# Kernel optimization log

Hardware: AMD Instinct MI355X
Metric: run time of the kernel (lower is better)

Reference implementation:

```python
import jax, jax.numpy as jnp
import numpy as np

LOG2PI = float(np.log(2.0 * np.pi))
T, DZ, DX = 512, 32, 32  # dx == dz so all quad forms stack homogeneously


def _spd(key, d):
    a = jax.random.normal(key, (d, d))
    return a @ a.T / d + jnp.eye(d)


def setup_inputs() -> dict:
    key = jax.random.key(0)
    k = jax.random.split(key, 17)
    return {
        "observations": jax.random.normal(k[0], (T, DX)),
        "m_prior_mean": jax.random.normal(k[1], (DZ,)),
        "m_prior_cov": _spd(k[2], DZ),
        "m_trans_w": 0.3 * jax.random.normal(k[3], (DZ, DZ)),
        "m_trans_b": jax.random.normal(k[4], (DZ,)),
        "m_trans_cov": _spd(k[5], DZ),
        "m_emis_w": 0.3 * jax.random.normal(k[6], (DX, DZ)),
        "m_emis_b": jax.random.normal(k[7], (DX,)),
        "m_emis_cov": _spd(k[8], DX),
        "v_prior_mean": jax.random.normal(k[9], (DZ,)),
        "v_prior_cov": _spd(k[10], DZ),
        "v_trans_w": 0.3 * jax.random.normal(k[11], (DZ, DZ)),
        "v_trans_b": jax.random.normal(k[12], (DZ,)),
        "v_trans_cov": _spd(k[13], DZ),
        "v_emis_w": 0.3 * jax.random.normal(k[14], (DX, DZ)),
        "v_emis_b": jax.random.normal(k[15], (DX,)),
        "v_emis_cov": _spd(k[16], DX),
    }


def _elbo(observations, m_prior_mean, m_prior_cov, m_trans_w, m_trans_b,
          m_trans_cov, m_emis_w, m_emis_b, m_emis_cov, v_prior_mean,
          v_prior_cov, v_trans_w, v_trans_b, v_trans_cov, v_emis_w,
          v_emis_b, v_emis_cov):
    Tn, dx = observations.shape
    dz = m_trans_cov.shape[0]
    I = jnp.eye(dz, dtype=observations.dtype)

    def logdet(M):
        return jnp.log(jnp.linalg.det(M))

    def cterm(dim, ld):  # -0.5*(dim*log(2pi) + log det)
        return -0.5 * (dim * LOG2PI + ld)

    m_trans_prec = jnp.linalg.inv(m_trans_cov)
    m_trans_ld = logdet(m_trans_cov)
    m_emis_prec = jnp.linalg.inv(m_emis_cov)
    m_emis_ld = logdet(m_emis_cov)
    v_trans_prec = jnp.linalg.inv(v_trans_cov)

    # ---- Kalman filter on the variational model ----
    def kf_update(m, P, y):
        S = v_emis_w @ P @ v_emis_w.T + v_emis_cov
        K = P @ v_emis_w.T @ jnp.linalg.inv(S)
        m2 = m + K @ (y - (v_emis_w @ m + v_emis_b))
        P2 = (I - K @ v_emis_w) @ P
        return m2, P2

    def kf_step(m, P, y):
        mp = v_trans_w @ m + v_trans_b
        Pp = v_trans_w @ P @ v_trans_w.T + v_trans_cov
        return kf_update(mp, Pp, y)

    # ---- stacked quad forms; list grows by 2 per step -> 2T slots ----
    N = 2 * Tn
    Om = jnp.zeros((N, dz, dz), observations.dtype)
    A = jnp.zeros((N, dz, dz), observations.dtype)
    b = jnp.zeros((N, dz), observations.dtype)
    # slot 0: emission/obs term at t=0
    Om = Om.at[0].set(-0.5 * m_emis_prec)
    A = A.at[0].set(m_emis_w)
    b = b.at[0].set(m_emis_b - observations[0])
    # slot 1: prior term
    Om = Om.at[1].set(-0.5 * jnp.linalg.inv(m_prior_cov))
    A = A.at[1].set(I)
    b = b.at[1].set(-m_prior_mean)

    fm, fP = kf_update(v_prior_mean, v_prior_cov, observations[0])
    c0 = cterm(dz, logdet(m_prior_cov)) + cterm(dx, m_emis_ld)

    def step(carry, xs):
        fm, fP, c, Om, A, b = carry
        t, y = xs
        # backward kernel from current filtering state
        fprec = jnp.linalg.inv(fP)
        common = v_trans_w.T @ v_trans_prec
        bcov = jnp.linalg.inv(common @ v_trans_w + fprec)
        bA = bcov @ common
        ba = bcov @ (fprec @ fm - common @ v_trans_b)
        # integrate all existing quad forms under the backward kernel
        # (zero slots contribute exactly 0, so no masking is needed)
        AbC = jnp.einsum('nij,jk->nik', A, bcov)
        c = c + jnp.sum(jnp.einsum('nab,nbc,nac->n', Om, AbC, A))
        A2 = jnp.einsum('nij,jk->nik', A, bA)
        b2 = jnp.einsum('nij,j->ni', A, ba) + b
        c = c + cterm(dx, m_emis_ld) + cterm(dz, m_trans_ld)
        # transition quad form expectation constant
        c = c - 0.5 * jnp.trace(m_trans_prec @ m_trans_w @ bcov @ m_trans_w.T)
        # append obs term (slot 2t) and transition term (slot 2t+1)
        Om2 = Om.at[2 * t].set(-0.5 * m_emis_prec).at[2 * t + 1].set(-0.5 * m_trans_prec)
        A2 = A2.at[2 * t].set(m_emis_w).at[2 * t + 1].set(m_trans_w @ bA - I)
        b2 = b2.at[2 * t].set(m_emis_b - y).at[2 * t + 1].set(m_trans_w @ ba + m_trans_b)
        # backward entropy constant + 0.5*dz
        c = c - cterm(dz, logdet(bcov)) + 0.5 * dz
        fm2, fP2 = kf_step(fm, fP, y)
        return (fm2, fP2, c, Om2, A2, b2), None

    ts = jnp.arange(1, Tn)
    (fm, fP, c, Om, A, b), _ = jax.lax.scan(
        step, (fm, fP, c0, Om, A, b), (ts, observations[1:]))

    # final expectations under the filtering distribution
    c = c - cterm(dz, logdet(fP))
    # trace(Omega @ A @ fP @ A)  -- note A (not A.T), faithful to the source
    tr = jnp.einsum('nab,nbc,cd,nda->n', Om, A, fP, A)
    cm = jnp.einsum('nij,j->ni', A, fm) + b
    qf = jnp.einsum('ni,nij,nj->n', cm, Om, cm)
    c = c + jnp.sum(tr) + jnp.sum(qf) + 0.5 * dz
    return c


def reference(observations, m_prior_mean, m_prior_cov, m_trans_w, m_trans_b,
              m_trans_cov, m_emis_w, m_emis_b, m_emis_cov, v_prior_mean,
              v_prior_cov, v_trans_w, v_trans_b, v_trans_cov, v_emis_w,
              v_emis_b, v_emis_cov):
    return _elbo(observations, m_prior_mean, m_prior_cov, m_trans_w,
                 m_trans_b, m_trans_cov, m_emis_w, m_emis_b, m_emis_cov,
                 v_prior_mean, v_prior_cov, v_trans_w, v_trans_b,
                 v_trans_cov, v_emis_w, v_emis_b, v_emis_cov)
```

## Files before the change

### kernel.cpp

```cpp
#include <hip/hip_runtime.h>
#include <math.h>

#define TT 512
#define CH 8
#define NCH 64
#define NB 128
#define NGRP 8
#define GSZ (NB/NGRP)
#define ST 36
#define MS 1152
#define LOG2PI 1.8378770664093453

static_assert(TT == CH * NCH, "chunking");

enum : int {
  WS_X     = 0,
  WS_BCOV  = WS_X    + TT*1024,
  WS_BA    = WS_BCOV + TT*1024,
  WS_YT    = WS_BA   + TT*32,
  WS_MTP   = WS_YT   + TT*32,
  WS_MEP   = WS_MTP + 1024,
  WS_MPP   = WS_MEP + 1024,
  WS_QI    = WS_MPP + 1024,
  WS_RI    = WS_QI  + 1024,
  WS_P0I   = WS_RI  + 1024,
  WS_QIW   = WS_P0I + 1024,
  WS_CW    = WS_QIW + 1024,
  WS_HTRI  = WS_CW  + 1024,
  WS_HTRIH = WS_HTRI+ 1024,
  WS_TQ    = WS_HTRIH+1024,
  WS_EM    = WS_TQ  + 1024,
  WS_EML   = WS_EM  + 1024,
  WS_LAM0CW= WS_EML + 1024,
  WS_QHC   = WS_LAM0CW + 1024,
  WS_C1    = WS_QHC + 1024,
  WS_EMM   = WS_C1  + 1024,
  WS_S1    = WS_EMM + 1024,
  WS_FPT   = WS_S1  + 1024,
  WS_ETA0  = WS_FPT + 1024,
  WS_CTB   = WS_ETA0 + 32,
  WS_QIVTB = WS_CTB + 32,
  WS_FMT   = WS_QIVTB + 32,
  WS_ETAF  = WS_FMT + 32,
  WS_LDS3  = WS_ETAF + 32,
  WS_DACC  = WS_LDS3 + 4,
  WS_Z512  = WS_DACC + 8,
  WS_OPS   = WS_Z512 + 1024,
  WS_GBAR  = WS_OPS + 6*3072,
  WS_PART  = WS_GBAR + 4352,
  WS_ETA_A = WS_PART + 416,
  WS_ETA_B = WS_ETA_A + NCH*1056,
  WS_CEA   = WS_ETA_B + NCH*1056,
  WS_CEB   = WS_CEA + NCH*2048,
  WS_END   = WS_CEB + NCH*2048
};
static_assert(WS_DACC % 2 == 0 && WS_PART % 2 == 0, "double alignment");

__device__ __forceinline__ float rlane(float v, int l) {
  return __uint_as_float(__builtin_amdgcn_readlane(__float_as_uint(v), l));
}
__device__ __forceinline__ float dot4(const float4 a, const float4 b) {
  return a.x*b.x + a.y*b.y + a.z*b.z + a.w*b.w;
}

__device__ __forceinline__ double gj_inv32(float a[32]) {
  double pp = 1.0;
#pragma unroll
  for (int p = 0; p < 32; ++p) {
    const float piv = rlane(a[p], p);
    pp *= (double)piv;
    const float sc = a[p] * (1.0f / piv);
#pragma unroll
    for (int r = 0; r < 32; ++r) {
      if (r != p) a[r] -= rlane(a[r], p) * sc;
    }
    a[p] = sc;
  }
  return pp;
}

__device__ __forceinline__ double wave_inv36(float* M, int tid) {
  float a[32]; const int cc = tid & 31;
#pragma unroll
  for (int r = 0; r < 32; ++r)
    a[r] = (tid < 32) ? M[r*ST + cc] : ((r == tid - 32) ? 1.f : 0.f);
  const double pp = gj_inv32(a);
  if (tid >= 32) {
    const int c2 = tid - 32;
#pragma unroll
    for (int r = 0; r < 32; ++r) M[r*ST + c2] = a[r];
  }
  return pp;
}

__device__ __forceinline__ float block_reduce(float v, float* red, int tid) {
#pragma unroll
  for (int m = 32; m >= 1; m >>= 1) v += __shfl_xor(v, m, 64);
  if ((tid & 63) == 0) red[tid >> 6] = v;
  __syncthreads();
  return red[0] + red[1] + red[2] + red[3];
}

__device__ __forceinline__ void stage_mat(const float* __restrict__ g, float* L, int tid) {
  const int r = tid >> 3, c = (tid & 7) * 4;
  *(float4*)(L + r*ST + c) = *(const float4*)(g + r*32 + c);
}
__device__ __forceinline__ void destage_mat(const float* L, float* __restrict__ g, int tid) {
  const int r = tid >> 3, c = (tid & 7) * 4;
  *(float4*)(g + r*32 + c) = *(const float4*)(L + r*ST + c);
}

__device__ __forceinline__ void mm_rr(const float* A, const float* B, float* C, int tid) {
  const int j = tid & 31, r0 = tid >> 5;
  float4 b[8];
#pragma unroll
  for (int kk = 0; kk < 8; ++kk) b[kk] = *(const float4*)(B + j*ST + 4*kk);
#pragma unroll
  for (int m = 0; m < 4; ++m) {
    const int ri = r0 + 8*m;
    float s = 0.f;
#pragma unroll
    for (int kk = 0; kk < 8; ++kk)
      s += dot4(*(const float4*)(A + ri*ST + 4*kk), b[kk]);
    C[ri*ST+j] = s;
  }
}
__device__ __forceinline__ void mm_rr_sub(const float* A, const float* B,
                                          const float* Base, float* C, int tid) {
  const int j = tid & 31, r0 = tid >> 5;
  float4 b[8];
#pragma unroll
  for (int kk = 0; kk < 8; ++kk) b[kk] = *(const float4*)(B + j*ST + 4*kk);
#pragma unroll
  for (int m = 0; m < 4; ++m) {
    const int ri = r0 + 8*m;
    float s = 0.f;
#pragma unroll
    for (int kk = 0; kk < 8; ++kk)
      s += dot4(*(const float4*)(A + ri*ST + 4*kk), b[kk]);
    C[ri*ST+j] = Base[ri*ST+j] - s;
  }
}
__device__ __forceinline__ void mm_rr_subg(const float* A, const float* B,
                                           const float* __restrict__ gBase,
                                           float* C, int tid) {
  const int j = tid & 31, r0 = tid >> 5;
  float4 b[8];
#pragma unroll
  for (int kk = 0; kk < 8; ++kk) b[kk] = *(const float4*)(B + j*ST + 4*kk);
#pragma unroll
  for (int m = 0; m < 4; ++m) {
    const int ri = r0 + 8*m;
    float s = 0.f;
#pragma unroll
    for (int kk = 0; kk < 8; ++kk)
      s += dot4(*(const float4*)(A + ri*ST + 4*kk), b[kk]);
    C[ri*ST+j] = gBase[ri*32+j] - s;
  }
}
__device__ __forceinline__ void mm_p(const float* A, const float* B, float* C, int tid) {
  const int ri = tid >> 3, j4 = (tid & 7) * 4;
  float4 acc = {0.f,0.f,0.f,0.f};
#pragma unroll 8
  for (int k = 0; k < 32; ++k) {
    const float a = A[ri*ST + k];
    const float4 b = *(const float4*)(B + k*ST + j4);
    acc.x += a*b.x; acc.y += a*b.y; acc.z += a*b.z; acc.w += a*b.w;
  }
  *(float4*)(C + ri*ST + j4) = acc;
}
__device__ __forceinline__ void mm_p_sub(const float* A, const float* B,
                                         const float* Base, float* C, int tid) {
  const int ri = tid >> 3, j4 = (tid & 7) * 4;
  float4 acc = *(const float4*)(Base + ri*ST + j4);
#pragma unroll 8
  for (int k = 0; k < 32; ++k) {
    const float a = A[ri*ST + k];
    const float4 b = *(const float4*)(B + k*ST + j4);
    acc.x -= a*b.x; acc.y -= a*b.y; acc.z -= a*b.z; acc.w -= a*b.w;
  }
  *(float4*)(C + ri*ST + j4) = acc;
}
__device__ __forceinline__ void mm_tp(const float* A, const float* B, float* C, int tid) {
  const int ri = tid >> 3, j4 = (tid & 7) * 4;
  float4 acc = {0.f,0.f,0.f,0.f};
#pragma unroll 8
  for (int k = 0; k < 32; ++k) {
    const float a = A[k*ST + ri];
    const float4 b = *(const float4*)(B + k*ST + j4);
    acc.x += a*b.x; acc.y += a*b.y; acc.z += a*b.z; acc.w += a*b.w;
  }
  *(float4*)(C + ri*ST + j4) = acc;
}
__device__ __forceinline__ void mm_tp_addL(const float* A, const float* B,
                                           const float* AddL, float* C, int tid) {
  const int ri = tid >> 3, j4 = (tid & 7) * 4;
  float4 acc = *(const float4*)(AddL + ri*ST + j4);
#pragma unroll 8
  for (int k = 0; k < 32; ++k) {
    const float a = A[k*ST + ri];
    const float4 b = *(const float4*)(B + k*ST + j4);
    acc.x += a*b.x; acc.y += a*b.y; acc.z += a*b.z; acc.w += a*b.w;
  }
  *(float4*)(C + ri*ST + j4) = acc;
}

__device__ __forceinline__ void gridbar(unsigned* base, int idx, int blk) {
  __syncthreads();
  if (threadIdx.x == 0) {
    const int g = blk & (NGRP-1);
    unsigned* lcl  = base + idx*128 + g*16;
    unsigned* go   = base + 2048 + idx*128 + g*16;
    unsigned* glob = base + 4096 + idx*16;
    __threadfence();
    __hip_atomic_fetch_add(lcl, 1u, __ATOMIC_RELEASE, __HIP_MEMORY_SCOPE_AGENT);
    if (blk < NGRP) {
      while (__hip_atomic_load(lcl, __ATOMIC_ACQUIRE, __HIP_MEMORY_SCOPE_AGENT)
             < (unsigned)GSZ)
        __builtin_amdgcn_s_sleep(1);
      __hip_atomic_fetch_add(glob, 1u, __ATOMIC_RELEASE, __HIP_MEMORY_SCOPE_AGENT);
      while (__hip_atomic_load(glob, __ATOMIC_ACQUIRE, __HIP_MEMORY_SCOPE_AGENT)
             < (unsigned)NGRP)
        __builtin_amdgcn_s_sleep(1);
      __hip_atomic_store(go, 1u, __ATOMIC_RELEASE, __HIP_MEMORY_SCOPE_AGENT);
    } else {
      while (__hip_atomic_load(go, __ATOMIC_ACQUIRE, __HIP_MEMORY_SCOPE_AGENT) == 0u)
        __builtin_amdgcn_s_sleep(1);
    }
  }
  __syncthreads();
}

__device__ void dev_k2(const float* __restrict__ obs, const float* __restrict__ vpm,
                       const float* __restrict__ vtw, const float* __restrict__ vtb,
                       const float* __restrict__ vew, const float* __restrict__ veb,
                       const float* __restrict__ mtw, const float* __restrict__ mew,
                       float* __restrict__ ws, int tid) {
  const int j = tid & 31, r0 = tid >> 5;
#pragma unroll
  for (int m = 0; m < 4; ++m) {
    const int ri = r0 + 8*m;
    float s1 = 0.f, s2 = 0.f, s3 = 0.f, s4 = 0.f;
    for (int k = 0; k < 32; ++k) {
      s1 += ws[WS_QI  + ri*32 + k] * vtw[k*32 + j];
      s2 += vew[k*32 + ri] * ws[WS_RI + k*32 + j];
      s3 += ws[WS_MTP + ri*32 + k] * mtw[k*32 + j];
      s4 += ws[WS_MEP + ri*32 + k] * mew[k*32 + j];
    }
    ws[WS_QIW + ri*32 + j] = s1;
    ws[WS_HTRI + ri*32 + j] = s2;
    ws[WS_FPT + ri*32 + j] = s3;
    ws[WS_EML + ri*32 + j] = -0.5f * s4;
  }
  __syncthreads();
#pragma unroll
  for (int m = 0; m < 4; ++m) {
    const int ri = r0 + 8*m;
    float s1 = 0.f, s2 = 0.f, s3 = 0.f, s4 = 0.f;
    for (int k = 0; k < 32; ++k) {
      s1 += vtw[k*32 + ri] * ws[WS_QIW + k*32 + j];
      s2 += ws[WS_HTRI + ri*32 + k] * vew[k*32 + j];
      s3 += mtw[k*32 + ri] * ws[WS_FPT + k*32 + j];
      s4 += mew[k*32 + ri] * ws[WS_EML + k*32 + j];
    }
    ws[WS_CW + ri*32 + j] = s1;
    ws[WS_HTRIH + ri*32 + j] = s2;
    ws[WS_LAM0CW + ri*32 + j] = ws[WS_P0I + ri*32 + j] + s1 + s2;
    ws[WS_QHC    + ri*32 + j] = ws[WS_QI  + ri*32 + j] + s1 + s2;
    ws[WS_TQ + ri*32 + j] = s3;
    ws[WS_EM + ri*32 + j] = s4;
    ws[WS_S1 + ri*32 + j] = s4 - 0.5f * ws[WS_MPP + ri*32 + j];
    ws[WS_C1 + ri*32 + j] = ws[WS_FPT + j*32 + ri];
    ws[WS_EMM + ri*32 + j] = s4 - 0.5f * ws[WS_MTP + ri*32 + j];
  }
  if (tid < 32) {
    float s1 = 0.f, s2 = 0.f, s3 = 0.f;
    for (int k = 0; k < 32; ++k) {
      s1 += ws[WS_QIW + k*32 + tid] * vtb[k];
      s2 += ws[WS_P0I + tid*32 + k] * vpm[k]
          + ws[WS_HTRI + tid*32 + k] * (obs[k] - veb[k]);
      s3 += ws[WS_QI + tid*32 + k] * vtb[k];
    }
    ws[WS_CTB + tid] = s1;
    ws[WS_ETA0 + tid] = s2;
    ws[WS_QIVTB + tid] = s3;
  }
  __syncthreads();
  if (tid == 0) {
    const double ldmt = (double)ws[WS_LDS3 + 0];
    const double ldme = (double)ws[WS_LDS3 + 1];
    const double ldmp = (double)ws[WS_LDS3 + 2];
    const double ct_me = -0.5 * (32.0 * LOG2PI + ldme);
    const double ct_mt = -0.5 * (32.0 * LOG2PI + ldmt);
    const double ct_mp = -0.5 * (32.0 * LOG2PI + ldmp);
    double c = ct_mp + ct_me;
    c += (double)(TT - 1) * (ct_me + ct_mt + 0.5 * 32.0 * LOG2PI + 16.0);
    c += 0.5 * 32.0 * LOG2PI + 16.0;
    ((double*)(ws + WS_DACC))[0] = c;
  }
  __syncthreads();
}

__device__ void dev_compose(float* __restrict__ ws, float* sm, int tid) {
  float *Kc = sm,      *Ac = sm+MS,   *Gc = sm+2*MS;
  float *Kn = sm+3*MS, *An = sm+4*MS, *Gn = sm+5*MS;
  float *Mi = sm+6*MS, *V1 = sm+7*MS, *Wm = sm+8*MS;
  stage_mat(ws + WS_QHC, Kc, tid);
  stage_mat(ws + WS_QIW, Ac, tid);
  for (int e = tid; e < MS; e += 256) Gc[e] = 0.f;
  __syncthreads();
  for (int d = 0; d < 8; ++d) {
    for (int e = tid; e < MS; e += 256) Mi[e] = Kc[e] + Gc[e];
    __syncthreads();
    if (tid < 64) wave_inv36(Mi, tid);
    __syncthreads();
    mm_rr(Ac, Mi, V1, tid);
    mm_tp(Ac, Mi, Wm, tid);
    __syncthreads();
    mm_rr_sub(V1, Ac, Kc, Kn, tid);
    mm_p(V1, Ac, An, tid);
    mm_p_sub(Wm, Ac, Gc, Gn, tid);
    __syncthreads();
    float* tp;
    tp=Kc; Kc=Kn; Kn=tp;  tp=Ac; Ac=An; An=tp;  tp=Gc; Gc=Gn; Gn=tp;
    if (d >= 2) {
      float* op = ws + WS_OPS + (d-2)*3072;
      destage_mat(Kc, op, tid);
      destage_mat(Ac, op + 1024, tid);
      destage_mat(Gc, op + 2048, tid);
    }
  }
}

__device__ void dev_keta_a(float* __restrict__ ws, float* sm, int tid, int c) {
  float *Aa = sm, *Ab = sm+MS, *Xl = sm+2*MS, *bb = sm+3*MS;
  const int t1 = CH*c + 1;
  stage_mat(ws + WS_X + t1*1024, Aa, tid);
  if (tid < 32) bb[tid] = ws[WS_YT + t1*32 + tid];
  __syncthreads();
  float *Acur = Aa, *Anew = Ab; int pb = 0;
  for (int t = t1 + 1; t <= t1 + CH - 1; ++t) {
    stage_mat(ws + WS_X + t*1024, Xl, tid);
    __syncthreads();
    mm_p(Xl, Acur, Anew, tid);
    if (tid < 32) {
      float s = ws[WS_YT + t*32 + tid];
      for (int k = 0; k < 32; ++k) s += Xl[tid*ST+k] * bb[pb*32 + k];
      bb[(pb^1)*32 + tid] = s;
    }
    __syncthreads();
    float* tp = Acur; Acur = Anew; Anew = tp; pb ^= 1;
  }
  float* dst = ws + WS_ETA_A + (c+1)*1056;
  destage_mat(Acur, dst, tid);
  if (tid < 32) dst[1024 + tid] = bb[pb*32 + tid];
}

__device__ void dev_eta_lvl8(float* __restrict__ ws, float* sm, int tid, int c) {
  const float* in = ws + WS_ETA_A;
  float* out = ws + WS_ETA_B;
  float *AR0 = sm, *AR1 = sm+MS, *A0 = sm+2*MS;
  float *bv = sm+3*MS, *b0 = bv + 64;
  stage_mat(in + c*1056, AR0, tid);
  if (tid < 32) bv[tid] = in[c*1056 + 1024 + tid];
  __syncthreads();
  float *AR = AR0, *At = AR1; int pb = 0;
  for (int kk = 1; kk <= 7; ++kk) {
    const int idx = c - kk;
    if (idx < 0) break;
    stage_mat(in + idx*1056, A0, tid);
    if (tid < 32) b0[tid] = in[idx*1056 + 1024 + tid];
    __syncthreads();
    mm_p(AR, A0, At, tid);
    if (tid < 32) {
      float s = bv[pb*32 + tid];
      for (int k = 0; k < 32; ++k) s += AR[tid*ST+k] * b0[k];
      bv[(pb^1)*32 + tid] = s;
    }
    __syncthreads();
    float* tp = AR; AR = At; At = tp; pb ^= 1;
  }
  destage_mat(AR, out + c*1056, tid);
  if (tid < 32) out[c*1056 + 1024 + tid] = bv[pb*32 + tid];
}

__device__ void dev_keta_b(float* __restrict__ ws, float* sm, int tid, int c) {
  float *A_0 = sm, *A_1 = sm+MS, *A_2 = sm+2*MS;
  float *bb = sm+3*MS;
  stage_mat(ws + WS_ETA_B + c*1056, A_0, tid);
  if (tid < 32) bb[tid] = ws[WS_ETA_B + c*1056 + 1024 + tid];
  __syncthreads();
  float *AR = A_0, *Ax = A_1; int pb = 0;
  for (int kk = 1; kk <= 7; ++kk) {
    const int idx = c - 8*kk;
    if (idx < 0) break;
    stage_mat(ws + WS_ETA_B + idx*1056, A_2, tid);
    if (tid < 32) bb[64 + tid] = ws[WS_ETA_B + idx*1056 + 1024 + tid];
    __syncthreads();
    mm_p(AR, A_2, Ax, tid);
    if (tid < 32) {
      float s = bb[pb*32 + tid];
      for (int k = 0; k < 32; ++k) s += AR[tid*ST+k] * bb[64+k];
      bb[(pb^1)*32 + tid] = s;
    }
    __syncthreads();
    float* tp = AR; AR = Ax; Ax = tp; pb ^= 1;
  }
  float *zeta = bb + 96, *zn = bb + 128;
  if (tid < 32) {
    float s = bb[pb*32 + tid];
    for (int k = 0; k < 32; ++k)
      s += AR[tid*ST+k] * (ws[WS_ETA0 + k] - ws[WS_CTB + k]);
    zeta[tid] = s;
  }
  __syncthreads();
  float *Bl = A_0, *Xl = A_1;
  const int nst = (c == NCH-1) ? CH-1 : CH;
  for (int i = 0; i < nst; ++i) {
    const int t = CH*c + 1 + i;
    stage_mat(ws + WS_BCOV + t*1024, Bl, tid);
    stage_mat(ws + WS_X + t*1024, Xl, tid);
    __syncthreads();
    if (tid < 32) {
      float s = 0.f;
      for (int k = 0; k < 32; ++k) s += Bl[tid*ST+k] * zeta[k];
      ws[WS_BA + t*32 + tid] = s;
    } else if (tid < 64) {
      const int i2 = tid - 32;
      float s = ws[WS_YT + t*32 + i2];
      for (int k = 0; k < 32; ++k) s += Xl[i2*ST+k] * zeta[k];
      zn[i2] = s;
    }
    __syncthreads();
    if (tid < 32) zeta[tid] = zn[tid];
    __syncthreads();
  }
  if (c == NCH-1 && tid < 32)
    ws[WS_ETAF + tid] = zeta[tid] + ws[WS_CTB + tid];
}

__device__ void dev_ksa(float* __restrict__ ws, float* sm, int tid, int c) {
  float *BTa=sm,      *BTb=sm+MS,   *Ka=sm+2*MS,  *Kb=sm+3*MS,
        *Tk=sm+4*MS,  *XC1=sm+5*MS, *Xl=sm+6*MS,  *KmTQ=sm+7*MS,
        *TQl=sm+8*MS, *EMMl=sm+9*MS,*C1l=sm+10*MS;
  const int t1 = CH*c + 1, t2 = CH*c + CH;
  const int j = tid & 31, r0 = tid >> 5;
  stage_mat(ws + WS_TQ, TQl, tid);
  stage_mat(ws + WS_EMM, EMMl, tid);
  stage_mat(ws + WS_C1, C1l, tid);
  for (int e = tid; e < MS; e += 256) {
    const int r = e / ST, cc = e - ST*r;
    BTa[e] = (cc < 32 && cc == r) ? 1.f : 0.f;
    Ka[e] = 0.f;
  }
  __syncthreads();
  float *BTc = BTa, *BTn = BTb, *Kc = Ka, *Kn = Kb;
  for (int t = t1; t <= t2; ++t) {
    stage_mat(ws + WS_X + t*1024, Xl, tid);
    for (int e = tid; e < MS; e += 256) KmTQ[e] = Kc[e] - 0.5f * TQl[e];
    __syncthreads();
    mm_rr(BTc, Xl, BTn, tid);
    mm_rr(Xl, KmTQ, Tk, tid);
    mm_p(Xl, C1l, XC1, tid);
    __syncthreads();
    {
      float4 xb[8];
#pragma unroll
      for (int kk = 0; kk < 8; ++kk) xb[kk] = *(const float4*)(Xl + j*ST + 4*kk);
#pragma unroll
      for (int m = 0; m < 4; ++m) {
        const int ri = r0 + 8*m;
        float s = 0.f;
#pragma unroll
        for (int kk = 0; kk < 8; ++kk)
          s += dot4(*(const float4*)(Tk + ri*ST + 4*kk), xb[kk]);
        Kn[ri*ST+j] = s + 0.5f*(XC1[ri*ST+j] + XC1[j*ST+ri]) + EMMl[ri*ST+j];
      }
    }
    __syncthreads();
    float* tp = BTc; BTc = BTn; BTn = tp;
    tp = Kc; Kc = Kn; Kn = tp;
  }
  float* dst = ws + WS_CEA + (c+1)*2048;
  destage_mat(BTc, dst, tid);
  destage_mat(Kc, dst + 1024, tid);
}

__device__ void dev_ks_lvl8(float* __restrict__ ws, float* sm, int tid, int c) {
  const float* in = ws + WS_CEA;
  float* out = ws + WS_CEB;
  float *BT0=sm, *BT1=sm+MS, *K0=sm+2*MS, *K1=sm+3*MS,
        *BTo=sm+4*MS, *Ko=sm+5*MS, *tmp=sm+6*MS;
  stage_mat(in + c*2048, BT0, tid);
  stage_mat(in + c*2048 + 1024, K0, tid);
  __syncthreads();
  float *BTR=BT0, *BTt=BT1, *KR=K0, *Kt=K1;
  for (int kk = 1; kk <= 7; ++kk) {
    const int idx = c - kk;
    if (idx < 0) break;
    stage_mat(in + idx*2048, BTo, tid);
    stage_mat(in + idx*2048 + 1024, Ko, tid);
    __syncthreads();
    mm_p(Ko, BTR, tmp, tid);
    mm_p(BTo, BTR, BTt, tid);
    __syncthreads();
    mm_tp_addL(BTR, tmp, KR, Kt, tid);
    __syncthreads();
    float* tp = BTR; BTR = BTt; BTt = tp;
    tp = KR; KR = Kt; Kt = tp;
  }
  destage_mat(BTR, out + c*2048, tid);
  destage_mat(KR, out + c*2048 + 1024, tid);
}

__device__ void dev_ksc(float* __restrict__ ws, float* sm, float* red,
                        int tid, int c) {
  float *BT0=sm, *BT1=sm+MS, *K0=sm+2*MS, *K1=sm+3*MS,
        *BTo=sm+4*MS, *Ko=sm+5*MS, *tmp=sm+6*MS;
  stage_mat(ws + WS_CEB + c*2048, BT0, tid);
  stage_mat(ws + WS_CEB + c*2048 + 1024, K0, tid);
  __syncthreads();
  float *BTR=BT0, *BTt=BT1, *KR=K0, *Kt=K1;
  for (int kk = 1; kk <= 7; ++kk) {
    const int idx = c - 8*kk;
    if (idx < 0) break;
    stage_mat(ws + WS_CEB + idx*2048, BTo, tid);
    stage_mat(ws + WS_CEB + idx*2048 + 1024, Ko, tid);
    __syncthreads();
    mm_p(Ko, BTR, tmp, tid);
    mm_p(BTo, BTR, BTt, tid);
    __syncthreads();
    mm_tp_addL(BTR, tmp, KR, Kt, tid);
    __syncthreads();
    float* tp = BTR; BTR = BTt; BTt = tp;
    tp = KR; KR = Kt; Kt = tp;
  }
  float *TQl=sm+7*MS, *EMMl=sm+8*MS, *C1l=sm+9*MS,
        *S=sm+10*MS, *SmTQ=sm+11*MS, *XC1=sm+12*MS;
  float *T1=tmp, *Xl=BTo, *Bcl=Ko;
  const int j = tid & 31, r0 = tid >> 5;
  stage_mat(ws + WS_TQ, TQl, tid);
  stage_mat(ws + WS_EMM, EMMl, tid);
  stage_mat(ws + WS_C1, C1l, tid);
  stage_mat(ws + WS_S1, SmTQ, tid);
  __syncthreads();
  mm_p(SmTQ, BTR, T1, tid);
  __syncthreads();
  mm_tp_addL(BTR, T1, KR, S, tid);
  __syncthreads();
  double accd = 0.0;
  for (int i = 0; i < CH; ++i) {
    const int t = CH*c + 1 + i;
    if (t >= TT) break;
    stage_mat(ws + WS_X + t*1024, Xl, tid);
    stage_mat(ws + WS_BCOV + t*1024, Bcl, tid);
#pragma unroll
    for (int m = 0; m < 4; ++m) {
      const int ri = r0 + 8*m;
      SmTQ[ri*ST+j] = S[ri*ST+j] - 0.5f * TQl[ri*ST+j];
    }
    __syncthreads();
    float part = 0.f;
#pragma unroll
    for (int m = 0; m < 4; ++m) {
      const int ri = r0 + 8*m;
      part += SmTQ[ri*ST+j] * Bcl[ri*ST+j];
    }
    const float r2 = block_reduce(part, red, tid);
    if (tid == 0) accd += (double)r2;
    mm_rr(Xl, SmTQ, T1, tid);
    mm_p(Xl, C1l, XC1, tid);
    __syncthreads();
    {
      float4 xb[8];
#pragma unroll
      for (int kk = 0; kk < 8; ++kk) xb[kk] = *(const float4*)(Xl + j*ST + 4*kk);
#pragma unroll
      for (int m = 0; m < 4; ++m) {
        const int ri = r0 + 8*m;
        float s = 0.f;
#pragma unroll
        for (int kk = 0; kk < 8; ++kk)
          s += dot4(*(const float4*)(T1 + ri*ST + 4*kk), xb[kk]);
        S[ri*ST+j] = s + 0.5f*(XC1[ri*ST+j] + XC1[j*ST+ri]) + EMMl[ri*ST+j];
      }
    }
    __syncthreads();
  }
  if (tid == 0) ((double*)(ws + WS_PART))[64 + c] = accd;
}

__device__ void dev_kga(float* __restrict__ ws, float* sm, int tid, int c) {
  float *ATa = sm, *ATb = sm+MS, *Xl = sm+2*MS, *bb = sm+3*MS;
  const int t1 = CH*c + 1;
  const int t2 = (CH*c + CH < TT) ? CH*c + CH : TT - 1;
  stage_mat(ws + WS_X + t2*1024, ATa, tid);
  if (tid < 32) bb[tid] = ws[WS_BA + t2*32 + tid];
  __syncthreads();
  float *ATc = ATa, *ATn = ATb;
  int pb = 0;
  for (int t = t2 - 1; t >= t1; --t) {
    stage_mat(ws + WS_X + t*1024, Xl, tid);
    __syncthreads();
    mm_p(ATc, Xl, ATn, tid);
    if (tid < 32) {
      float s = ws[WS_BA + t*32 + tid];
      for (int k = 0; k < 32; ++k) s += Xl[k*ST+tid] * bb[pb*32 + k];
      bb[(pb^1)*32 + tid] = s;
    }
    __syncthreads();
    float* tp = ATc; ATc = ATn; ATn = tp; pb ^= 1;
  }
  float* dst = ws + WS_CEA + (c-1)*1056;
  destage_mat(ATc, dst, tid);
  if (tid < 32) dst[1024 + tid] = bb[pb*32 + tid];
}

__device__ void dev_kg_lvl8(float* __restrict__ ws, float* sm, int tid, int c) {
  const float* in = ws + WS_CEA;
  float* out = ws + WS_CEB;
  float *AR0 = sm, *AR1 = sm+MS, *ATl = sm+2*MS;
  float *bv = sm+3*MS, *bl = bv + 64;
  stage_mat(in + c*1056, AR0, tid);
  if (tid < 32) bv[tid] = in[c*1056 + 1024 + tid];
  __syncthreads();
  float *AR = AR0, *At = AR1; int pb = 0;
  for (int kk = 1; kk <= 7; ++kk) {
    const int idx = c + kk;
    if (idx > NCH - 1) break;
    stage_mat(in + idx*1056, ATl, tid);
    if (tid < 32) bl[tid] = in[idx*1056 + 1024 + tid];
    __syncthreads();
    mm_p(ATl, AR, At, tid);
    if (tid < 32) {
      float s = bv[pb*32 + tid];
      for (int k = 0; k < 32; ++k) s += AR[k*ST+tid] * bl[k];
      bv[(pb^1)*32 + tid] = s;
    }
    __syncthreads();
    float* tp = AR; AR = At; At = tp; pb ^= 1;
  }
  destage_mat(AR, out + c*1056, tid);
  if (tid < 32) out[c*1056 + 1024 + tid] = bv[pb*32 + tid];
}

__device__ void dev_kgb(const float* __restrict__ obs, const float* __restrict__ mpm,
                        const float* __restrict__ mtw, const float* __restrict__ mtb,
                        const float* __restrict__ mew, const float* __restrict__ meb,
                        float* __restrict__ ws, float* sm, float* red, int tid, int c) {
  float *ATa=sm,      *ATb=sm+MS,    *Xl=sm+2*MS,  *Y1=sm+3*MS,  *Y2=sm+4*MS,
        *Jb=sm+5*MS,  *M2T=sm+6*MS,  *mewl=sm+7*MS,*EmLl=sm+8*MS,
        *fPl=sm+9*MS, *Mtpl=sm+10*MS,*Mepl=sm+11*MS,*mtwl=sm+12*MS;
  float *vec = sm + 13*MS;
  float *fml=vec, *mebl=vec+32, *mtbl=vec+64, *mpml=vec+96, *yl=vec+128,
        *bal=vec+160, *gv=vec+192, *cme=vec+224, *cmo=vec+256, *bv=vec+288;
  const int j = tid & 31, r0 = tid >> 5;
  stage_mat(mew, mewl, tid);
  stage_mat(ws + WS_EML, EmLl, tid);
  stage_mat(ws + WS_FPT, fPl, tid);
  stage_mat(ws + WS_MTP, Mtpl, tid);
  stage_mat(ws + WS_MEP, Mepl, tid);
  stage_mat(mtw, mtwl, tid);
  stage_mat(ws + WS_CEB + c*1056, ATa, tid);
  if (tid < 32) {
    fml[tid] = ws[WS_FMT + tid];
    mebl[tid] = meb[tid]; mtbl[tid] = mtb[tid]; mpml[tid] = mpm[tid];
    bv[tid] = ws[WS_CEB + c*1056 + 1024 + tid];
  }
  __syncthreads();
  float *ATc = ATa, *ATo = ATb;
  int bc = 0;
  for (int kk = 1; kk <= 7; ++kk) {
    const int idx = c + 8*kk;
    if (idx > NCH - 1) break;
    stage_mat(ws + WS_CEB + idx*1056, Xl, tid);
    if (tid < 32) bal[tid] = ws[WS_CEB + idx*1056 + 1024 + tid];
    __syncthreads();
    mm_p(Xl, ATc, ATo, tid);
    if (tid < 32) {
      float s = bv[bc*32 + tid];
      for (int k = 0; k < 32; ++k) s += ATc[k*ST+tid] * bal[k];
      bv[(bc^1)*32 + tid] = s;
    }
    __syncthreads();
    float* tp = ATc; ATc = ATo; ATo = tp; bc ^= 1;
  }
  double accd = 0.0;
  for (int s = CH*c + CH - 1; s >= CH*c; --s) {
    if (s < TT-1) stage_mat(ws + WS_X + (s+1)*1024, Xl, tid);
    if (s == 0)   stage_mat(ws + WS_MPP, Jb, tid);
    if (tid < 32) {
      yl[tid] = obs[s*32 + tid];
      if (s >= 1) bal[tid] = ws[WS_BA + s*32 + tid];
    }
    __syncthreads();
    if (s < TT-1) {
      mm_p(ATc, Xl, ATo, tid);
      if (tid < 32) {
        float v = ws[WS_BA + (s+1)*32 + tid];
        for (int k = 0; k < 32; ++k) v += Xl[k*ST+tid] * bv[bc*32 + k];
        bv[(bc^1)*32 + tid] = v;
      }
    }
    __syncthreads();
    const float* AT = (s < TT-1) ? ATo : ATc;
    const float* bl = (s < TT-1) ? (bv + (bc^1)*32) : (bv + bc*32);
    mm_rr(mewl, AT, Y1, tid);
    mm_rr(EmLl, AT, Y2, tid);
    if (s >= 1) {
      const float* Xg = ws + WS_X + s*1024;
      float4 xg[8];
#pragma unroll
      for (int kk = 0; kk < 8; ++kk) xg[kk] = *(const float4*)(Xg + j*32 + 4*kk);
#pragma unroll
      for (int m = 0; m < 4; ++m) {
        const int ri = r0 + 8*m;
        float v = 0.f;
#pragma unroll
        for (int kk = 0; kk < 8; ++kk)
          v += dot4(*(const float4*)(mtwl + ri*ST + 4*kk), xg[kk]);
        Jb[ri*ST+j] = v - ((ri == j) ? 1.f : 0.f);
      }
    }
    if (tid < 32) {
      float g = bl[tid];
      for (int k = 0; k < 32; ++k) g += AT[k*ST+tid] * fml[k];
      gv[tid] = g;
    }
    __syncthreads();
    if (s >= 1) mm_rr(AT, Jb, M2T, tid);
    if (tid < 32) {
      float s1v = mebl[tid] - yl[tid];
      for (int k = 0; k < 32; ++k) s1v += mewl[tid*ST+k] * gv[k];
      cme[tid] = s1v;
      float s2v;
      if (s >= 1) {
        s2v = mtbl[tid];
        for (int k = 0; k < 32; ++k)
          s2v += Jb[tid*ST+k] * gv[k] + mtwl[tid*ST+k] * bal[k];
      } else {
        s2v = gv[tid] - mpml[tid];
      }
      cmo[tid] = s2v;
    }
    __syncthreads();
    const float* M2Tp = (s >= 1) ? M2T : AT;
    const float* Mqp  = (s >= 1) ? Mtpl : Jb;
    float4 fb[8], m2b[8];
#pragma unroll
    for (int kk = 0; kk < 8; ++kk) {
      fb[kk]  = *(const float4*)(fPl + j*ST + 4*kk);
      m2b[kk] = *(const float4*)(M2Tp + j*ST + 4*kk);
    }
    float part = 0.f;
#pragma unroll
    for (int m = 0; m < 4; ++m) {
      const int ri = r0 + 8*m;
      float y3 = 0.f, e2 = 0.f, e1 = 0.f;
#pragma unroll
      for (int kk = 0; kk < 8; ++kk) {
        y3 += dot4(*(const float4*)(Y2 + ri*ST + 4*kk), fb[kk]);
        e2 += dot4(fb[kk], *(const float4*)(M2Tp + ri*ST + 4*kk));
        e1 += dot4(*(const float4*)(Mqp + ri*ST + 4*kk), m2b[kk]);
      }
      part += y3 * Y1[j*ST+ri]
            - 0.5f * e1 * e2
            - 0.5f * cme[ri] * Mepl[ri*ST+j] * cme[j]
            - 0.5f * cmo[ri] * Mqp[ri*ST+j] * cmo[j];
    }
    const float r2 = block_reduce(part, red, tid);
    if (tid == 0) accd += (double)r2;
    if (s < TT-1) { float* tp = ATc; ATc = ATo; ATo = tp; bc ^= 1; }
    __syncthreads();
  }
  if (tid == 0) ((double*)(ws + WS_PART))[128 + c] = accd;
}

__global__ __launch_bounds__(256) void k0_init(float* __restrict__ ws) {
  unsigned* b = (unsigned*)(ws + WS_GBAR);
  for (int e = threadIdx.x; e < 4352; e += 256) b[e] = 0u;
}

__global__ __launch_bounds__(256) void mega(
    const float* __restrict__ obs, const float* __restrict__ mpm,
    const float* __restrict__ mpc, const float* __restrict__ mtw,
    const float* __restrict__ mtb, const float* __restrict__ mtc,
    const float* __restrict__ mew, const float* __restrict__ meb,
    const float* __restrict__ mec, const float* __restrict__ vpm,
    const float* __restrict__ vpc, const float* __restrict__ vtw,
    const float* __restrict__ vtb, const float* __restrict__ vtc,
    const float* __restrict__ vew, const float* __restrict__ veb,
    const float* __restrict__ vcc, float* __restrict__ ws,
    float* __restrict__ out) {
  __shared__ __align__(16) float sm[15360];
  __shared__ float red[4];
  const int tid = threadIdx.x, blk = blockIdx.x;
  unsigned* bars = (unsigned*)(ws + WS_GBAR);
  double* P = (double*)(ws + WS_PART);
  int bix = 0;

  if (blk < 6) {
    const float* src = blk==0?mtc : blk==1?mec : blk==2?mpc : blk==3?vtc : blk==4?vcc : vpc;
    float* dst = ws + (blk==0?WS_MTP : blk==1?WS_MEP : blk==2?WS_MPP :
                       blk==3?WS_QI  : blk==4?WS_RI  : WS_P0I);
    if (tid < 64) {
      float a[32]; const int cc = tid & 31;
#pragma unroll
      for (int r = 0; r < 32; ++r)
        a[r] = (tid < 32) ? src[r*32 + cc] : ((r == tid - 32) ? 1.f : 0.f);
      const double pp = gj_inv32(a);
      if (tid >= 32) {
        const int c2 = tid - 32;
#pragma unroll
        for (int r = 0; r < 32; ++r) dst[r*32 + c2] = a[r];
      }
      if (tid == 0 && blk < 3) ws[WS_LDS3 + blk] = (float)log(pp);
    }
  }
  gridbar(bars, bix++, blk);

  if (blk == 0) {
    dev_k2(obs, vpm, vtw, vtb, vew, veb, mtw, mew, ws, tid);
    dev_compose(ws, sm, tid);
  }
  gridbar(bars, bix++, blk);

  if (blk < NCH) {
    float *Zl=sm, *Mi=sm+MS, *Aol=sm+2*MS, *V1=sm+3*MS;
    float *Bcv=sm+4*MS, *Xs=sm+5*MS, *QiWl=sm+6*MS, *QHCl=sm+7*MS;
    const int c = blk;
    stage_mat(ws + WS_LAM0CW, Zl, tid);
    stage_mat(ws + WS_QIW, QiWl, tid);
    stage_mat(ws + WS_QHC, QHCl, tid);
    __syncthreads();
    for (int k = 0; k < 6; ++k) {
      if (!((c >> k) & 1)) continue;
      const float* OP = ws + WS_OPS + k*3072;
      {
        const int r = tid >> 3, c4 = (tid & 7) * 4;
        const float4 g = *(const float4*)(OP + 2048 + r*32 + c4);
        float4 z = *(const float4*)(Zl + r*ST + c4);
        z.x += g.x; z.y += g.y; z.z += g.z; z.w += g.w;
        *(float4*)(Mi + r*ST + c4) = z;
      }
      stage_mat(OP + 1024, Aol, tid);
      __syncthreads();
      if (tid < 64) wave_inv36(Mi, tid);
      __syncthreads();
      mm_rr(Aol, Mi, V1, tid);
      __syncthreads();
      mm_rr_subg(V1, Aol, OP, Zl, tid);
      __syncthreads();
    }
    const int nst = (c == NCH-1) ? CH-1 : CH;
    double acc = 0.0;
    for (int i = 0; i < nst; ++i) {
      const int t = CH*c + 1 + i;
      if (tid < 64) {
        float a[32]; const int cc = tid & 31;
#pragma unroll
        for (int r = 0; r < 32; ++r)
          a[r] = (tid < 32) ? Zl[r*ST+cc] : ((r == tid - 32) ? 1.f : 0.f);
        const double pp = gj_inv32(a);
        if (tid >= 32) {
          const int c2 = tid - 32;
#pragma unroll
          for (int r = 0; r < 32; ++r) {
            Bcv[r*ST + c2] = a[r];
            ws[WS_BCOV + t*1024 + r*32 + c2] = a[r];
          }
        }
        if (tid == 0) acc += -log(pp);
      }
      __syncthreads();
      mm_rr(QiWl, Bcv, Xs, tid);
      __syncthreads();
      destage_mat(Xs, ws + WS_X + t*1024, tid);
      mm_rr_sub(Xs, QiWl, QHCl, Zl, tid);
      __syncthreads();
    }
    if (c == NCH-1) destage_mat(Zl, ws + WS_Z512, tid);
    if (tid == 0) P[blk] = acc;
  } else {
    const int tb = blk - NCH;
    const int t = tb*CH + (tid >> 5), i = tid & 31;
    float s = ws[WS_QIVTB + i] - ws[WS_CTB + i];
    for (int k = 0; k < 32; ++k)
      s += ws[WS_HTRI + i*32 + k] * (obs[t*32 + k] - veb[k]);
    ws[WS_YT + t*32 + i] = s;
  }
  gridbar(bars, bix++, blk);

  if (blk < NCH) {
    if (blk < NCH-1) {
      dev_keta_a(ws, sm, tid, blk);
    } else {
      for (int e = tid; e < 1056; e += 256)
        ws[WS_ETA_A + e] = (e < 1024 && ((e >> 5) == (e & 31))) ? 1.f : 0.f;
    }
  } else {
    const int c = blk - NCH;
    if (c < NCH-1) {
      dev_ksa(ws, sm, tid, c);
    } else {
      for (int e = tid; e < 2048; e += 256)
        ws[WS_CEA + e] = (e < 1024 && ((e >> 5) == (e & 31))) ? 1.f : 0.f;
    }
  }
  gridbar(bars, bix++, blk);

  if (blk < NCH) dev_eta_lvl8(ws, sm, tid, blk);
  else           dev_ks_lvl8(ws, sm, tid, blk - NCH);
  gridbar(bars, bix++, blk);

  if (blk < NCH) {
    dev_keta_b(ws, sm, tid, blk);
    __threadfence();
    __syncthreads();
    if (blk == 0) {
      for (int e = tid; e < 1056; e += 256)
        ws[WS_CEA + (NCH-1)*1056 + e] =
            (e < 1024 && ((e >> 5) == (e & 31))) ? 1.f : 0.f;
    } else {
      dev_kga(ws, sm, tid, blk);
    }
  } else {
    dev_ksc(ws, sm, red, tid, blk - NCH);
  }
  gridbar(bars, bix++, blk);

  if (blk < NCH) {
    dev_kg_lvl8(ws, sm, tid, blk);
  } else if (blk == NCH) {
    if (tid < 64) {
      float a[32]; const int cc = tid & 31;
#pragma unroll
      for (int r = 0; r < 32; ++r) {
        const float v = ws[WS_Z512 + r*32 + cc] - ws[WS_CW + r*32 + cc];
        a[r] = (tid < 32) ? v : ((r == tid - 32) ? 1.f : 0.f);
      }
      const double pp = gj_inv32(a);
      if (tid >= 32) {
        const int c2 = tid - 32;
        float fmv = 0.f;
#pragma unroll
        for (int r = 0; r < 32; ++r) {
          ws[WS_FPT + r*32 + c2] = a[r];
          fmv += a[r] * ws[WS_ETAF + r];
        }
        ws[WS_FMT + c2] = fmv;
      }
      if (tid == 0) P[192] = -log(pp);
    }
  }
  gridbar(bars, bix++, blk);

  if (blk < NCH) dev_kgb(obs, mpm, mtw, mtb, mew, meb, ws, sm, red, tid, blk);
  gridbar(bars, bix++, blk);

  if (blk == 0 && tid < 64) {
    double v = 0.5 * P[tid] + P[64 + tid] + P[128 + tid];
#pragma unroll
    for (int m = 32; m >= 1; m >>= 1) v += __shfl_xor(v, m, 64);
    if (tid == 0) {
      const double* d = (const double*)(ws + WS_DACC);
      out[0] = (float)(v + d[0] + 0.5 * P[192]);
    }
  }
}

extern "C" void kernel_launch(void* const* d_in, const int* in_sizes, int n_in,
                              void* d_out, int out_size, void* d_ws, size_t ws_size,
                              hipStream_t stream) {
  (void)in_sizes; (void)n_in; (void)out_size; (void)ws_size;
  const float* obs = (const float*)d_in[0];
  const float* mpm = (const float*)d_in[1];
  const float* mpc = (const float*)d_in[2];
  const float* mtw = (const float*)d_in[3];
  const float* mtb = (const float*)d_in[4];
  const float* mtc = (const float*)d_in[5];
  const float* mew = (const float*)d_in[6];
  const float* meb = (const float*)d_in[7];
  const float* mec = (const float*)d_in[8];
  const float* vpm = (const float*)d_in[9];
  const float* vpc = (const float*)d_in[10];
  const float* vtw = (const float*)d_in[11];
  const float* vtb = (const float*)d_in[12];
  const float* vtc = (const float*)d_in[13];
  const float* vew = (const float*)d_in[14];
  const float* veb = (const float*)d_in[15];
  const float* vcc = (const float*)d_in[16];
  float* ws  = (float*)d_ws;
  float* out = (float*)d_out;

  k0_init<<<1, 256, 0, stream>>>(ws);
  mega<<<NB, 256, 0, stream>>>(obs, mpm, mpc, mtw, mtb, mtc, mew, meb, mec,
                               vpm, vpc, vtw, vtb, vtc, vew, veb, vcc, ws, out);
}
```

Before: 606.3 us.

## Compute each 32x32 matmul per-wave with 4x4 register tiles and run independent products concurrently

Replaces the block-wide 32x32 matmul helpers with single-wave versions where each lane computes a 4x4 output tile from float4 LDS loads, using a rotated k-order to spread LDS bank accesses. Independent matrix products in each step are assigned to different waves so they run concurrently instead of one after another across the whole block. The aim is more register-level reuse and less LDS traffic per FLOP on the latency-bound sequential chain. In exchange, some waves sit idle during single-product phases and each lane holds more registers.

```diff
diff --git a/kernel.cpp b/kernel.cpp
--- a/kernel.cpp
+++ b/kernel.cpp
@@ -62,6 +62,9 @@
 __device__ __forceinline__ float dot4(const float4 a, const float4 b) {
   return a.x*b.x + a.y*b.y + a.z*b.z + a.w*b.w;
 }
+__device__ __forceinline__ float f4c(const float4 v, int e) {
+  switch (e) { case 0: return v.x; case 1: return v.y; case 2: return v.z; default: return v.w; }
+}
 
 __device__ __forceinline__ double gj_inv32(float a[32]) {
   double pp = 1.0;
@@ -110,54 +113,6 @@
   *(float4*)(g + r*32 + c) = *(const float4*)(L + r*ST + c);
 }
 
-__device__ __forceinline__ void mm_rr(const float* A, const float* B, float* C, int tid) {
-  const int j = tid & 31, r0 = tid >> 5;
-  float4 b[8];
-#pragma unroll
-  for (int kk = 0; kk < 8; ++kk) b[kk] = *(const float4*)(B + j*ST + 4*kk);
-#pragma unroll
-  for (int m = 0; m < 4; ++m) {
-    const int ri = r0 + 8*m;
-    float s = 0.f;
-#pragma unroll
-    for (int kk = 0; kk < 8; ++kk)
-      s += dot4(*(const float4*)(A + ri*ST + 4*kk), b[kk]);
-    C[ri*ST+j] = s;
-  }
-}
-__device__ __forceinline__ void mm_rr_sub(const float* A, const float* B,
-                                          const float* Base, float* C, int tid) {
-  const int j = tid & 31, r0 = tid >> 5;
-  float4 b[8];
-#pragma unroll
-  for (int kk = 0; kk < 8; ++kk) b[kk] = *(const float4*)(B + j*ST + 4*kk);
-#pragma unroll
-  for (int m = 0; m < 4; ++m) {
-    const int ri = r0 + 8*m;
-    float s = 0.f;
-#pragma unroll
-    for (int kk = 0; kk < 8; ++kk)
-      s += dot4(*(const float4*)(A + ri*ST + 4*kk), b[kk]);
-    C[ri*ST+j] = Base[ri*ST+j] - s;
-  }
-}
-__device__ __forceinline__ void mm_rr_subg(const float* A, const float* B,
-                                           const float* __restrict__ gBase,
-                                           float* C, int tid) {
-  const int j = tid & 31, r0 = tid >> 5;
-  float4 b[8];
-#pragma unroll
-  for (int kk = 0; kk < 8; ++kk) b[kk] = *(const float4*)(B + j*ST + 4*kk);
-#pragma unroll
-  for (int m = 0; m < 4; ++m) {
-    const int ri = r0 + 8*m;
-    float s = 0.f;
-#pragma unroll
-    for (int kk = 0; kk < 8; ++kk)
-      s += dot4(*(const float4*)(A + ri*ST + 4*kk), b[kk]);
-    C[ri*ST+j] = gBase[ri*32+j] - s;
-  }
-}
 __device__ __forceinline__ void mm_p(const float* A, const float* B, float* C, int tid) {
   const int ri = tid >> 3, j4 = (tid & 7) * 4;
   float4 acc = {0.f,0.f,0.f,0.f};
@@ -169,40 +124,234 @@
   }
   *(float4*)(C + ri*ST + j4) = acc;
 }
-__device__ __forceinline__ void mm_p_sub(const float* A, const float* B,
-                                         const float* Base, float* C, int tid) {
-  const int ri = tid >> 3, j4 = (tid & 7) * 4;
-  float4 acc = *(const float4*)(Base + ri*ST + j4);
-#pragma unroll 8
-  for (int k = 0; k < 32; ++k) {
-    const float a = A[ri*ST + k];
-    const float4 b = *(const float4*)(B + k*ST + j4);
-    acc.x -= a*b.x; acc.y -= a*b.y; acc.z -= a*b.z; acc.w -= a*b.w;
-  }
-  *(float4*)(C + ri*ST + j4) = acc;
-}
-__device__ __forceinline__ void mm_tp(const float* A, const float* B, float* C, int tid) {
-  const int ri = tid >> 3, j4 = (tid & 7) * 4;
-  float4 acc = {0.f,0.f,0.f,0.f};
-#pragma unroll 8
-  for (int k = 0; k < 32; ++k) {
-    const float a = A[k*ST + ri];
-    const float4 b = *(const float4*)(B + k*ST + j4);
-    acc.x += a*b.x; acc.y += a*b.y; acc.z += a*b.z; acc.w += a*b.w;
-  }
-  *(float4*)(C + ri*ST + j4) = acc;
-}
-__device__ __forceinline__ void mm_tp_addL(const float* A, const float* B,
-                                           const float* AddL, float* C, int tid) {
-  const int ri = tid >> 3, j4 = (tid & 7) * 4;
-  float4 acc = *(const float4*)(AddL + ri*ST + j4);
-#pragma unroll 8
-  for (int k = 0; k < 32; ++k) {
-    const float a = A[k*ST + ri];
-    const float4 b = *(const float4*)(B + k*ST + j4);
-    acc.x += a*b.x; acc.y += a*b.y; acc.z += a*b.z; acc.w += a*b.w;
-  }
-  *(float4*)(C + ri*ST + j4) = acc;
+
+__device__ __forceinline__ void w44_rr(const float* A, const float* B, float* C, int lane) {
+  const int r0 = (lane >> 3) * 4, c0 = (lane & 7) * 4, o = lane & 7;
+  float acc[4][4] = {};
+#pragma unroll
+  for (int kk = 0; kk < 8; ++kk) {
+    const int k4 = 4 * ((kk + o) & 7);
+    float4 a[4], b[4];
+#pragma unroll
+    for (int i = 0; i < 4; ++i) a[i] = *(const float4*)(A + (r0+i)*ST + k4);
+#pragma unroll
+    for (int jj = 0; jj < 4; ++jj) b[jj] = *(const float4*)(B + (c0+jj)*ST + k4);
+#pragma unroll
+    for (int i = 0; i < 4; ++i)
+#pragma unroll
+      for (int jj = 0; jj < 4; ++jj) acc[i][jj] += dot4(a[i], b[jj]);
+  }
+#pragma unroll
+  for (int i = 0; i < 4; ++i)
+    *(float4*)(C + (r0+i)*ST + c0) =
+        make_float4(acc[i][0], acc[i][1], acc[i][2], acc[i][3]);
+}
+__device__ __forceinline__ void w44_rr_sub(const float* A, const float* B,
+                                           const float* Base, float* C, int lane) {
+  const int r0 = (lane >> 3) * 4, c0 = (lane & 7) * 4, o = lane & 7;
+  float acc[4][4] = {};
+#pragma unroll
+  for (int kk = 0; kk < 8; ++kk) {
+    const int k4 = 4 * ((kk + o) & 7);
+    float4 a[4], b[4];
+#pragma unroll
+    for (int i = 0; i < 4; ++i) a[i] = *(const float4*)(A + (r0+i)*ST + k4);
+#pragma unroll
+    for (int jj = 0; jj < 4; ++jj) b[jj] = *(const float4*)(B + (c0+jj)*ST + k4);
+#pragma unroll
+    for (int i = 0; i < 4; ++i)
+#pragma unroll
+      for (int jj = 0; jj < 4; ++jj) acc[i][jj] += dot4(a[i], b[jj]);
+  }
+#pragma unroll
+  for (int i = 0; i < 4; ++i) {
+    const float4 bs = *(const float4*)(Base + (r0+i)*ST + c0);
+    *(float4*)(C + (r0+i)*ST + c0) =
+        make_float4(bs.x - acc[i][0], bs.y - acc[i][1], bs.z - acc[i][2], bs.w - acc[i][3]);
+  }
+}
+__device__ __forceinline__ void w44_rr_subg(const float* A, const float* B,
+                                            const float* __restrict__ gBase,
+                                            float* C, int lane) {
+  const int r0 = (lane >> 3) * 4, c0 = (lane & 7) * 4, o = lane & 7;
+  float acc[4][4] = {};
+#pragma unroll
+  for (int kk = 0; kk < 8; ++kk) {
+    const int k4 = 4 * ((kk + o) & 7);
+    float4 a[4], b[4];
+#pragma unroll
+    for (int i = 0; i < 4; ++i) a[i] = *(const float4*)(A + (r0+i)*ST + k4);
+#pragma unroll
+    for (int jj = 0; jj < 4; ++jj) b[jj] = *(const float4*)(B + (c0+jj)*ST + k4);
+#pragma unroll
+    for (int i = 0; i < 4; ++i)
+#pragma unroll
+      for (int jj = 0; jj < 4; ++jj) acc[i][jj] += dot4(a[i], b[jj]);
+  }
+#pragma unroll
+  for (int i = 0; i < 4; ++i) {
+    const float4 bs = *(const float4*)(gBase + (r0+i)*32 + c0);
+    *(float4*)(C + (r0+i)*ST + c0) =
+        make_float4(bs.x - acc[i][0], bs.y - acc[i][1], bs.z - acc[i][2], bs.w - acc[i][3]);
+  }
+}
+__device__ __forceinline__ void w44_p(const float* A, const float* B, float* C, int lane) {
+  const int r0 = (lane >> 3) * 4, c0 = (lane & 7) * 4, o = lane & 7;
+  float acc[4][4] = {};
+#pragma unroll
+  for (int kk = 0; kk < 8; ++kk) {
+    const int k4 = 4 * ((kk + o) & 7);
+    float4 a[4];
+#pragma unroll
+    for (int i = 0; i < 4; ++i) a[i] = *(const float4*)(A + (r0+i)*ST + k4);
+#pragma unroll
+    for (int e = 0; e < 4; ++e) {
+      const float4 b = *(const float4*)(B + (k4+e)*ST + c0);
+#pragma unroll
+      for (int i = 0; i < 4; ++i) {
+        const float av = f4c(a[i], e);
+        acc[i][0] += av*b.x; acc[i][1] += av*b.y; acc[i][2] += av*b.z; acc[i][3] += av*b.w;
+      }
+    }
+  }
+#pragma unroll
+  for (int i = 0; i < 4; ++i)
+    *(float4*)(C + (r0+i)*ST + c0) =
+        make_float4(acc[i][0], acc[i][1], acc[i][2], acc[i][3]);
+}
+__device__ __forceinline__ void w44_p_sub(const float* A, const float* B,
+                                          const float* Base, float* C, int lane) {
+  const int r0 = (lane >> 3) * 4, c0 = (lane & 7) * 4, o = lane & 7;
+  float acc[4][4] = {};
+#pragma unroll
+  for (int kk = 0; kk < 8; ++kk) {
+    const int k4 = 4 * ((kk + o) & 7);
+    float4 a[4];
+#pragma unroll
+    for (int i = 0; i < 4; ++i) a[i] = *(const float4*)(A + (r0+i)*ST + k4);
+#pragma unroll
+    for (int e = 0; e < 4; ++e) {
+      const float4 b = *(const float4*)(B + (k4+e)*ST + c0);
+#pragma unroll
+      for (int i = 0; i < 4; ++i) {
+        const float av = f4c(a[i], e);
+        acc[i][0] += av*b.x; acc[i][1] += av*b.y; acc[i][2] += av*b.z; acc[i][3] += av*b.w;
+      }
+    }
+  }
+#pragma unroll
+  for (int i = 0; i < 4; ++i) {
+    const float4 bs = *(const float4*)(Base + (r0+i)*ST + c0);
+    *(float4*)(C + (r0+i)*ST + c0) =
+        make_float4(bs.x - acc[i][0], bs.y - acc[i][1], bs.z - acc[i][2], bs.w - acc[i][3]);
+  }
+}
+__device__ __forceinline__ void w44_tp(const float* A, const float* B, float* C, int lane) {
+  const int r0 = (lane >> 3) * 4, c0 = (lane & 7) * 4, o = lane & 7;
+  float acc[4][4] = {};
+#pragma unroll
+  for (int kk = 0; kk < 8; ++kk) {
+    const int k4 = 4 * ((kk + o) & 7);
+#pragma unroll
+    for (int e = 0; e < 4; ++e) {
+      const int k = k4 + e;
+      const float4 av = *(const float4*)(A + k*ST + r0);
+      const float4 bv = *(const float4*)(B + k*ST + c0);
+      acc[0][0] += av.x*bv.x; acc[0][1] += av.x*bv.y; acc[0][2] += av.x*bv.z; acc[0][3] += av.x*bv.w;
+      acc[1][0] += av.y*bv.x; acc[1][1] += av.y*bv.y; acc[1][2] += av.y*bv.z; acc[1][3] += av.y*bv.w;
+      acc[2][0] += av.z*bv.x; acc[2][1] += av.z*bv.y; acc[2][2] += av.z*bv.z; acc[2][3] += av.z*bv.w;
+      acc[3][0] += av.w*bv.x; acc[3][1] += av.w*bv.y; acc[3][2] += av.w*bv.z; acc[3][3] += av.w*bv.w;
+    }
+  }
+#pragma unroll
+  for (int i = 0; i < 4; ++i)
+    *(float4*)(C + (r0+i)*ST + c0) =
+        make_float4(acc[i][0], acc[i][1], acc[i][2], acc[i][3]);
+}
+__device__ __forceinline__ void w44_tp_addL(const float* A, const float* B,
+                                            const float* AddL, float* C, int lane) {
+  const int r0 = (lane >> 3) * 4, c0 = (lane & 7) * 4, o = lane & 7;
+  float acc[4][4] = {};
+#pragma unroll
+  for (int kk = 0; kk < 8; ++kk) {
+    const int k4 = 4 * ((kk + o) & 7);
+#pragma unroll
+    for (int e = 0; e < 4; ++e) {
+      const int k = k4 + e;
+      const float4 av = *(const float4*)(A + k*ST + r0);
+      const float4 bv = *(const float4*)(B + k*ST + c0);
+      acc[0][0] += av.x*bv.x; acc[0][1] += av.x*bv.y; acc[0][2] += av.x*bv.z; acc[0][3] += av.x*bv.w;
+      acc[1][0] += av.y*bv.x; acc[1][1] += av.y*bv.y; acc[1][2] += av.y*bv.z; acc[1][3] += av.y*bv.w;
+      acc[2][0] += av.z*bv.x; acc[2][1] += av.z*bv.y; acc[2][2] += av.z*bv.z; acc[2][3] += av.z*bv.w;
+      acc[3][0] += av.w*bv.x; acc[3][1] += av.w*bv.y; acc[3][2] += av.w*bv.z; acc[3][3] += av.w*bv.w;
+    }
+  }
+#pragma unroll
+  for (int i = 0; i < 4; ++i) {
+    const float4 ad = *(const float4*)(AddL + (r0+i)*ST + c0);
+    *(float4*)(C + (r0+i)*ST + c0) =
+        make_float4(ad.x + acc[i][0], ad.y + acc[i][1], ad.z + acc[i][2], ad.w + acc[i][3]);
+  }
+}
+__device__ __forceinline__ void w44_epi(const float* Tk, const float* X,
+                                        const float* XC1, const float* EMM,
+                                        float* C, int lane) {
+  const int r0 = (lane >> 3) * 4, c0 = (lane & 7) * 4, o = lane & 7;
+  float acc[4][4] = {};
+#pragma unroll
+  for (int kk = 0; kk < 8; ++kk) {
+    const int k4 = 4 * ((kk + o) & 7);
+    float4 a[4], b[4];
+#pragma unroll
+    for (int i = 0; i < 4; ++i) a[i] = *(const float4*)(Tk + (r0+i)*ST + k4);
+#pragma unroll
+    for (int jj = 0; jj < 4; ++jj) b[jj] = *(const float4*)(X + (c0+jj)*ST + k4);
+#pragma unroll
+    for (int i = 0; i < 4; ++i)
+#pragma unroll
+      for (int jj = 0; jj < 4; ++jj) acc[i][jj] += dot4(a[i], b[jj]);
+  }
+  float4 xt[4];
+#pragma unroll
+  for (int jj = 0; jj < 4; ++jj) xt[jj] = *(const float4*)(XC1 + (c0+jj)*ST + r0);
+#pragma unroll
+  for (int i = 0; i < 4; ++i) {
+    const float4 xc = *(const float4*)(XC1 + (r0+i)*ST + c0);
+    const float4 em = *(const float4*)(EMM + (r0+i)*ST + c0);
+    float4 v;
+    v.x = acc[i][0] + 0.5f*(xc.x + f4c(xt[0], i)) + em.x;
+    v.y = acc[i][1] + 0.5f*(xc.y + f4c(xt[1], i)) + em.y;
+    v.z = acc[i][2] + 0.5f*(xc.z + f4c(xt[2], i)) + em.z;
+    v.w = acc[i][3] + 0.5f*(xc.w + f4c(xt[3], i)) + em.w;
+    *(float4*)(C + (r0+i)*ST + c0) = v;
+  }
+}
+__device__ __forceinline__ void w44_jb(const float* mtwL, const float* __restrict__ Xg,
+                                       float* C, int lane) {
+  const int r0 = (lane >> 3) * 4, c0 = (lane & 7) * 4, o = lane & 7;
+  float acc[4][4] = {};
+#pragma unroll
+  for (int kk = 0; kk < 8; ++kk) {
+    const int k4 = 4 * ((kk + o) & 7);
+    float4 a[4], b[4];
+#pragma unroll
+    for (int i = 0; i < 4; ++i) a[i] = *(const float4*)(mtwL + (r0+i)*ST + k4);
+#pragma unroll
+    for (int jj = 0; jj < 4; ++jj) b[jj] = *(const float4*)(Xg + (c0+jj)*32 + k4);
+#pragma unroll
+    for (int i = 0; i < 4; ++i)
+#pragma unroll
+      for (int jj = 0; jj < 4; ++jj) acc[i][jj] += dot4(a[i], b[jj]);
+  }
+#pragma unroll
+  for (int i = 0; i < 4; ++i) {
+    float4 v = make_float4(acc[i][0], acc[i][1], acc[i][2], acc[i][3]);
+    v.x -= (r0+i == c0    ) ? 1.f : 0.f;
+    v.y -= (r0+i == c0 + 1) ? 1.f : 0.f;
+    v.z -= (r0+i == c0 + 2) ? 1.f : 0.f;
+    v.w -= (r0+i == c0 + 3) ? 1.f : 0.f;
+    *(float4*)(C + (r0+i)*ST + c0) = v;
+  }
 }
 
 __device__ __forceinline__ void gridbar(unsigned* base, int idx, int blk) {
@@ -305,6 +454,7 @@
   float *Kc = sm,      *Ac = sm+MS,   *Gc = sm+2*MS;
   float *Kn = sm+3*MS, *An = sm+4*MS, *Gn = sm+5*MS;
   float *Mi = sm+6*MS, *V1 = sm+7*MS, *Wm = sm+8*MS;
+  const int wv = tid >> 6, lane = tid & 63;
   stage_mat(ws + WS_QHC, Kc, tid);
   stage_mat(ws + WS_QIW, Ac, tid);
   for (int e = tid; e < MS; e += 256) Gc[e] = 0.f;
@@ -314,12 +464,12 @@
     __syncthreads();
     if (tid < 64) wave_inv36(Mi, tid);
     __syncthreads();
-    mm_rr(Ac, Mi, V1, tid);
-    mm_tp(Ac, Mi, Wm, tid);
-    __syncthreads();
-    mm_rr_sub(V1, Ac, Kc, Kn, tid);
-    mm_p(V1, Ac, An, tid);
-    mm_p_sub(Wm, Ac, Gc, Gn, tid);
+    if (wv == 0) w44_rr(Ac, Mi, V1, lane);
+    else if (wv == 1) w44_tp(Ac, Mi, Wm, lane);
+    __syncthreads();
+    if (wv == 0) w44_rr_sub(V1, Ac, Kc, Kn, lane);
+    else if (wv == 1) w44_p(V1, Ac, An, lane);
+    else if (wv == 2) w44_p_sub(Wm, Ac, Gc, Gn, lane);
     __syncthreads();
     float* tp;
     tp=Kc; Kc=Kn; Kn=tp;  tp=Ac; Ac=An; An=tp;  tp=Gc; Gc=Gn; Gn=tp;
@@ -444,7 +594,7 @@
         *Tk=sm+4*MS,  *XC1=sm+5*MS, *Xl=sm+6*MS,  *KmTQ=sm+7*MS,
         *TQl=sm+8*MS, *EMMl=sm+9*MS,*C1l=sm+10*MS;
   const int t1 = CH*c + 1, t2 = CH*c + CH;
-  const int j = tid & 31, r0 = tid >> 5;
+  const int wv = tid >> 6, lane = tid & 63;
   stage_mat(ws + WS_TQ, TQl, tid);
   stage_mat(ws + WS_EMM, EMMl, tid);
   stage_mat(ws + WS_C1, C1l, tid);
@@ -459,24 +609,11 @@
     stage_mat(ws + WS_X + t*1024, Xl, tid);
     for (int e = tid; e < MS; e += 256) KmTQ[e] = Kc[e] - 0.5f * TQl[e];
     __syncthreads();
-    mm_rr(BTc, Xl, BTn, tid);
-    mm_rr(Xl, KmTQ, Tk, tid);
-    mm_p(Xl, C1l, XC1, tid);
-    __syncthreads();
-    {
-      float4 xb[8];
-#pragma unroll
-      for (int kk = 0; kk < 8; ++kk) xb[kk] = *(const float4*)(Xl + j*ST + 4*kk);
-#pragma unroll
-      for (int m = 0; m < 4; ++m) {
-        const int ri = r0 + 8*m;
-        float s = 0.f;
-#pragma unroll
-        for (int kk = 0; kk < 8; ++kk)
-          s += dot4(*(const float4*)(Tk + ri*ST + 4*kk), xb[kk]);
-        Kn[ri*ST+j] = s + 0.5f*(XC1[ri*ST+j] + XC1[j*ST+ri]) + EMMl[ri*ST+j];
-      }
-    }
+    if (wv == 0) w44_rr(BTc, Xl, BTn, lane);
+    else if (wv == 1) w44_rr(Xl, KmTQ, Tk, lane);
+    else if (wv == 2) w44_p(Xl, C1l, XC1, lane);
+    __syncthreads();
+    if (wv == 0) w44_epi(Tk, Xl, XC1, EMMl, Kn, lane);
     __syncthreads();
     float* tp = BTc; BTc = BTn; BTn = tp;
     tp = Kc; Kc = Kn; Kn = tp;
@@ -491,6 +628,7 @@
   float* out = ws + WS_CEB;
   float *BT0=sm, *BT1=sm+MS, *K0=sm+2*MS, *K1=sm+3*MS,
         *BTo=sm+4*MS, *Ko=sm+5*MS, *tmp=sm+6*MS;
+  const int wv = tid >> 6, lane = tid & 63;
   stage_mat(in + c*2048, BT0, tid);
   stage_mat(in + c*2048 + 1024, K0, tid);
   __syncthreads();
@@ -501,10 +639,10 @@
     stage_mat(in + idx*2048, BTo, tid);
     stage_mat(in + idx*2048 + 1024, Ko, tid);
     __syncthreads();
-    mm_p(Ko, BTR, tmp, tid);
-    mm_p(BTo, BTR, BTt, tid);
-    __syncthreads();
-    mm_tp_addL(BTR, tmp, KR, Kt, tid);
+    if (wv == 0) w44_p(Ko, BTR, tmp, lane);
+    else if (wv == 1) w44_p(BTo, BTR, BTt, lane);
+    __syncthreads();
+    if (wv == 0) w44_tp_addL(BTR, tmp, KR, Kt, lane);
     __syncthreads();
     float* tp = BTR; BTR = BTt; BTt = tp;
     tp = KR; KR = Kt; Kt = tp;
@@ -517,6 +655,7 @@
                         int tid, int c) {
   float *BT0=sm, *BT1=sm+MS, *K0=sm+2*MS, *K1=sm+3*MS,
         *BTo=sm+4*MS, *Ko=sm+5*MS, *tmp=sm+6*MS;
+  const int wv = tid >> 6, lane = tid & 63;
   stage_mat(ws + WS_CEB + c*2048, BT0, tid);
   stage_mat(ws + WS_CEB + c*2048 + 1024, K0, tid);
   __syncthreads();
@@ -527,10 +666,10 @@
     stage_mat(ws + WS_CEB + idx*2048, BTo, tid);
     stage_mat(ws + WS_CEB + idx*2048 + 1024, Ko, tid);
     __syncthreads();
-    mm_p(Ko, BTR, tmp, tid);
-    mm_p(BTo, BTR, BTt, tid);
-    __syncthreads();
-    mm_tp_addL(BTR, tmp, KR, Kt, tid);
+    if (wv == 0) w44_p(Ko, BTR, tmp, lane);
+    else if (wv == 1) w44_p(BTo, BTR, BTt, lane);
+    __syncthreads();
+    if (wv == 0) w44_tp_addL(BTR, tmp, KR, Kt, lane);
     __syncthreads();
     float* tp = BTR; BTR = BTt; BTt = tp;
     tp = KR; KR = Kt; Kt = tp;
@@ -538,15 +677,15 @@
   float *TQl=sm+7*MS, *EMMl=sm+8*MS, *C1l=sm+9*MS,
         *S=sm+10*MS, *SmTQ=sm+11*MS, *XC1=sm+12*MS;
   float *T1=tmp, *Xl=BTo, *Bcl=Ko;
-  const int j = tid & 31, r0 = tid >> 5;
+  const int j = tid & 31, r0q = tid >> 5;
   stage_mat(ws + WS_TQ, TQl, tid);
   stage_mat(ws + WS_EMM, EMMl, tid);
   stage_mat(ws + WS_C1, C1l, tid);
   stage_mat(ws + WS_S1, SmTQ, tid);
   __syncthreads();
-  mm_p(SmTQ, BTR, T1, tid);
-  __syncthreads();
-  mm_tp_addL(BTR, T1, KR, S, tid);
+  if (wv == 0) w44_p(SmTQ, BTR, T1, lane);
+  __syncthreads();
+  if (wv == 0) w44_tp_addL(BTR, T1, KR, S, lane);
   __syncthreads();
   double accd = 0.0;
   for (int i = 0; i < CH; ++i) {
@@ -556,35 +695,22 @@
     stage_mat(ws + WS_BCOV + t*1024, Bcl, tid);
 #pragma unroll
     for (int m = 0; m < 4; ++m) {
-      const int ri = r0 + 8*m;
+      const int ri = r0q + 8*m;
       SmTQ[ri*ST+j] = S[ri*ST+j] - 0.5f * TQl[ri*ST+j];
     }
     __syncthreads();
     float part = 0.f;
 #pragma unroll
     for (int m = 0; m < 4; ++m) {
-      const int ri = r0 + 8*m;
+      const int ri = r0q + 8*m;
       part += SmTQ[ri*ST+j] * Bcl[ri*ST+j];
     }
     const float r2 = block_reduce(part, red, tid);
     if (tid == 0) accd += (double)r2;
-    mm_rr(Xl, SmTQ, T1, tid);
-    mm_p(Xl, C1l, XC1, tid);
-    __syncthreads();
-    {
-      float4 xb[8];
-#pragma unroll
-      for (int kk = 0; kk < 8; ++kk) xb[kk] = *(const float4*)(Xl + j*ST + 4*kk);
-#pragma unroll
-      for (int m = 0; m < 4; ++m) {
-        const int ri = r0 + 8*m;
-        float s = 0.f;
-#pragma unroll
-        for (int kk = 0; kk < 8; ++kk)
-          s += dot4(*(const float4*)(T1 + ri*ST + 4*kk), xb[kk]);
-        S[ri*ST+j] = s + 0.5f*(XC1[ri*ST+j] + XC1[j*ST+ri]) + EMMl[ri*ST+j];
-      }
-    }
+    if (wv == 0) w44_rr(Xl, SmTQ, T1, lane);
+    else if (wv == 1) w44_p(Xl, C1l, XC1, lane);
+    __syncthreads();
+    if (wv == 0) w44_epi(T1, Xl, XC1, EMMl, S, lane);
     __syncthreads();
   }
   if (tid == 0) ((double*)(ws + WS_PART))[64 + c] = accd;
@@ -621,6 +747,7 @@
   float* out = ws + WS_CEB;
   float *AR0 = sm, *AR1 = sm+MS, *ATl = sm+2*MS;
   float *bv = sm+3*MS, *bl = bv + 64;
+  const int wv = tid >> 6, lane = tid & 63;
   stage_mat(in + c*1056, AR0, tid);
   if (tid < 32) bv[tid] = in[c*1056 + 1024 + tid];
   __syncthreads();
@@ -631,11 +758,11 @@
     stage_mat(in + idx*1056, ATl, tid);
     if (tid < 32) bl[tid] = in[idx*1056 + 1024 + tid];
     __syncthreads();
-    mm_p(ATl, AR, At, tid);
-    if (tid < 32) {
-      float s = bv[pb*32 + tid];
-      for (int k = 0; k < 32; ++k) s += AR[k*ST+tid] * bl[k];
-      bv[(pb^1)*32 + tid] = s;
+    if (wv == 0) w44_p(ATl, AR, At, lane);
+    else if (wv == 1 && lane < 32) {
+      float s = bv[pb*32 + lane];
+      for (int k = 0; k < 32; ++k) s += AR[k*ST+lane] * bl[k];
+      bv[(pb^1)*32 + lane] = s;
     }
     __syncthreads();
     float* tp = AR; AR = At; At = tp; pb ^= 1;
@@ -654,7 +781,7 @@
   float *vec = sm + 13*MS;
   float *fml=vec, *mebl=vec+32, *mtbl=vec+64, *mpml=vec+96, *yl=vec+128,
         *bal=vec+160, *gv=vec+192, *cme=vec+224, *cmo=vec+256, *bv=vec+288;
-  const int j = tid & 31, r0 = tid >> 5;
+  const int wv = tid >> 6, lane = tid & 63;
   stage_mat(mew, mewl, tid);
   stage_mat(ws + WS_EML, EmLl, tid);
   stage_mat(ws + WS_FPT, fPl, tid);
@@ -676,11 +803,11 @@
     stage_mat(ws + WS_CEB + idx*1056, Xl, tid);
     if (tid < 32) bal[tid] = ws[WS_CEB + idx*1056 + 1024 + tid];
     __syncthreads();
-    mm_p(Xl, ATc, ATo, tid);
-    if (tid < 32) {
-      float s = bv[bc*32 + tid];
-      for (int k = 0; k < 32; ++k) s += ATc[k*ST+tid] * bal[k];
-      bv[(bc^1)*32 + tid] = s;
+    if (wv == 0) w44_p(Xl, ATc, ATo, lane);
+    else if (wv == 3 && lane < 32) {
+      float s = bv[bc*32 + lane];
+      for (int k = 0; k < 32; ++k) s += ATc[k*ST+lane] * bal[k];
+      bv[(bc^1)*32 + lane] = s;
     }
     __syncthreads();
     float* tp = ATc; ATc = ATo; ATo = tp; bc ^= 1;
@@ -689,46 +816,32 @@
   for (int s = CH*c + CH - 1; s >= CH*c; --s) {
     if (s < TT-1) stage_mat(ws + WS_X + (s+1)*1024, Xl, tid);
     if (s == 0)   stage_mat(ws + WS_MPP, Jb, tid);
-    if (tid < 32) {
-      yl[tid] = obs[s*32 + tid];
-      if (s >= 1) bal[tid] = ws[WS_BA + s*32 + tid];
+    if (wv == 3 && lane < 32) {
+      yl[lane] = obs[s*32 + lane];
+      if (s >= 1) bal[lane] = ws[WS_BA + s*32 + lane];
     }
     __syncthreads();
     if (s < TT-1) {
-      mm_p(ATc, Xl, ATo, tid);
-      if (tid < 32) {
-        float v = ws[WS_BA + (s+1)*32 + tid];
-        for (int k = 0; k < 32; ++k) v += Xl[k*ST+tid] * bv[bc*32 + k];
-        bv[(bc^1)*32 + tid] = v;
+      if (wv == 0) w44_p(ATc, Xl, ATo, lane);
+      else if (wv == 3 && lane < 32) {
+        float v = ws[WS_BA + (s+1)*32 + lane];
+        for (int k = 0; k < 32; ++k) v += Xl[k*ST+lane] * bv[bc*32 + k];
+        bv[(bc^1)*32 + lane] = v;
       }
     }
+    if (s >= 1 && wv == 1) w44_jb(mtwl, ws + WS_X + s*1024, Jb, lane);
     __syncthreads();
     const float* AT = (s < TT-1) ? ATo : ATc;
     const float* bl = (s < TT-1) ? (bv + (bc^1)*32) : (bv + bc*32);
-    mm_rr(mewl, AT, Y1, tid);
-    mm_rr(EmLl, AT, Y2, tid);
-    if (s >= 1) {
-      const float* Xg = ws + WS_X + s*1024;
-      float4 xg[8];
-#pragma unroll
-      for (int kk = 0; kk < 8; ++kk) xg[kk] = *(const float4*)(Xg + j*32 + 4*kk);
-#pragma unroll
-      for (int m = 0; m < 4; ++m) {
-        const int ri = r0 + 8*m;
-        float v = 0.f;
-#pragma unroll
-        for (int kk = 0; kk < 8; ++kk)
-          v += dot4(*(const float4*)(mtwl + ri*ST + 4*kk), xg[kk]);
-        Jb[ri*ST+j] = v - ((ri == j) ? 1.f : 0.f);
-      }
-    }
-    if (tid < 32) {
-      float g = bl[tid];
-      for (int k = 0; k < 32; ++k) g += AT[k*ST+tid] * fml[k];
-      gv[tid] = g;
-    }
-    __syncthreads();
-    if (s >= 1) mm_rr(AT, Jb, M2T, tid);
+    if (wv == 0) w44_rr(mewl, AT, Y1, lane);
+    else if (wv == 1) w44_rr(EmLl, AT, Y2, lane);
+    else if (wv == 2) { if (s >= 1) w44_rr(AT, Jb, M2T, lane); }
+    else if (lane < 32) {
+      float g = bl[lane];
+      for (int k = 0; k < 32; ++k) g += AT[k*ST+lane] * fml[k];
+      gv[lane] = g;
+    }
+    __syncthreads();
     if (tid < 32) {
       float s1v = mebl[tid] - yl[tid];
       for (int k = 0; k < 32; ++k) s1v += mewl[tid*ST+k] * gv[k];
@@ -746,27 +859,68 @@
     __syncthreads();
     const float* M2Tp = (s >= 1) ? M2T : AT;
     const float* Mqp  = (s >= 1) ? Mtpl : Jb;
-    float4 fb[8], m2b[8];
-#pragma unroll
-    for (int kk = 0; kk < 8; ++kk) {
-      fb[kk]  = *(const float4*)(fPl + j*ST + 4*kk);
-      m2b[kk] = *(const float4*)(M2Tp + j*ST + 4*kk);
-    }
     float part = 0.f;
-#pragma unroll
-    for (int m = 0; m < 4; ++m) {
-      const int ri = r0 + 8*m;
-      float y3 = 0.f, e2 = 0.f, e1 = 0.f;
-#pragma unroll
-      for (int kk = 0; kk < 8; ++kk) {
-        y3 += dot4(*(const float4*)(Y2 + ri*ST + 4*kk), fb[kk]);
-        e2 += dot4(fb[kk], *(const float4*)(M2Tp + ri*ST + 4*kk));
-        e1 += dot4(*(const float4*)(Mqp + ri*ST + 4*kk), m2b[kk]);
+    {
+      const int r0 = (lane >> 3) * 4, c0 = (lane & 7) * 4, o = lane & 7;
+      if (wv == 0) {
+        float acc[4][4] = {};
+#pragma unroll
+        for (int kk = 0; kk < 8; ++kk) {
+          const int k4 = 4 * ((kk + o) & 7);
+          float4 a[4], b[4];
+#pragma unroll
+          for (int i = 0; i < 4; ++i) a[i] = *(const float4*)(Y2 + (r0+i)*ST + k4);
+#pragma unroll
+          for (int jj = 0; jj < 4; ++jj) b[jj] = *(const float4*)(fPl + (c0+jj)*ST + k4);
+#pragma unroll
+          for (int i = 0; i < 4; ++i)
+#pragma unroll
+            for (int jj = 0; jj < 4; ++jj) acc[i][jj] += dot4(a[i], b[jj]);
+        }
+#pragma unroll
+        for (int jj = 0; jj < 4; ++jj) {
+          const float4 y1t = *(const float4*)(Y1 + (c0+jj)*ST + r0);
+          part += acc[0][jj]*y1t.x + acc[1][jj]*y1t.y + acc[2][jj]*y1t.z + acc[3][jj]*y1t.w;
+        }
+      } else if (wv == 1) {
+        float e1[4][4] = {}, e2[4][4] = {};
+#pragma unroll
+        for (int kk = 0; kk < 8; ++kk) {
+          const int k4 = 4 * ((kk + o) & 7);
+          float4 mq[4], m2r[4], m2c[4], fp[4];
+#pragma unroll
+          for (int i = 0; i < 4; ++i) {
+            mq[i]  = *(const float4*)(Mqp  + (r0+i)*ST + k4);
+            m2r[i] = *(const float4*)(M2Tp + (r0+i)*ST + k4);
+          }
+#pragma unroll
+          for (int jj = 0; jj < 4; ++jj) {
+            m2c[jj] = *(const float4*)(M2Tp + (c0+jj)*ST + k4);
+            fp[jj]  = *(const float4*)(fPl  + (c0+jj)*ST + k4);
+          }
+#pragma unroll
+          for (int i = 0; i < 4; ++i)
+#pragma unroll
+            for (int jj = 0; jj < 4; ++jj) {
+              e1[i][jj] += dot4(mq[i], m2c[jj]);
+              e2[i][jj] += dot4(fp[jj], m2r[i]);
+            }
+        }
+#pragma unroll
+        for (int i = 0; i < 4; ++i)
+#pragma unroll
+          for (int jj = 0; jj < 4; ++jj) part -= 0.5f * e1[i][jj] * e2[i][jj];
+      } else if (wv == 2) {
+#pragma unroll
+        for (int i = 0; i < 4; ++i) {
+          const float4 me = *(const float4*)(Mepl + (r0+i)*ST + c0);
+          const float4 mq = *(const float4*)(Mqp  + (r0+i)*ST + c0);
+          part -= 0.5f * cme[r0+i] *
+                  (me.x*cme[c0] + me.y*cme[c0+1] + me.z*cme[c0+2] + me.w*cme[c0+3]);
+          part -= 0.5f * cmo[r0+i] *
+                  (mq.x*cmo[c0] + mq.y*cmo[c0+1] + mq.z*cmo[c0+2] + mq.w*cmo[c0+3]);
+        }
       }
-      part += y3 * Y1[j*ST+ri]
-            - 0.5f * e1 * e2
-            - 0.5f * cme[ri] * Mepl[ri*ST+j] * cme[j]
-            - 0.5f * cmo[ri] * Mqp[ri*ST+j] * cmo[j];
     }
     const float r2 = block_reduce(part, red, tid);
     if (tid == 0) accd += (double)r2;
@@ -795,6 +949,7 @@
   __shared__ __align__(16) float sm[15360];
   __shared__ float red[4];
   const int tid = threadIdx.x, blk = blockIdx.x;
+  const int wv = tid >> 6, lane = tid & 63;
   unsigned* bars = (unsigned*)(ws + WS_GBAR);
   double* P = (double*)(ws + WS_PART);
   int bix = 0;
@@ -847,9 +1002,9 @@
       __syncthreads();
       if (tid < 64) wave_inv36(Mi, tid);
       __syncthreads();
-      mm_rr(Aol, Mi, V1, tid);
+      if (wv == 0) w44_rr(Aol, Mi, V1, lane);
       __syncthreads();
-      mm_rr_subg(V1, Aol, OP, Zl, tid);
+      if (wv == 0) w44_rr_subg(V1, Aol, OP, Zl, lane);
       __syncthreads();
     }
     const int nst = (c == NCH-1) ? CH-1 : CH;
@@ -873,10 +1028,10 @@
         if (tid == 0) acc += -log(pp);
       }
       __syncthreads();
-      mm_rr(QiWl, Bcv, Xs, tid);
+      if (wv == 0) w44_rr(QiWl, Bcv, Xs, lane);
       __syncthreads();
       destage_mat(Xs, ws + WS_X + t*1024, tid);
-      mm_rr_sub(Xs, QiWl, QHCl, Zl, tid);
+      if (wv == 0) w44_rr_sub(Xs, QiWl, QHCl, Zl, lane);
       __syncthreads();
     }
     if (c == NCH-1) destage_mat(Zl, ws + WS_Z512, tid);
```

Result: slower. 647.5 us (+6.8%).
